# Kernel optimization log

Measured on AMD Instinct MI355X. Metric: run time of the kernel, lower is better.

## Reference

```python
import jax, jax.numpy as jnp
import numpy as np

NEG_INF = -1e9  # module uses -1e9 negativeInfinity constant
BS, DA, SL, H = 16, 512, 1024, 8


def setup_inputs() -> dict:
    key = jax.random.key(0)
    ks = jax.random.split(key, 8)
    return {
        "q":    jax.random.normal(ks[0], (BS, DA, SL), dtype=jnp.float32),
        "k_in": jax.random.normal(ks[1], (BS, DA, SL), dtype=jnp.float32),
        "v_in": jax.random.normal(ks[2], (BS, DA, SL), dtype=jnp.float32),
        "k_w":  jax.random.normal(ks[3], (DA, DA), dtype=jnp.float32) * 0.05,
        "k_b":  jax.random.normal(ks[4], (DA,), dtype=jnp.float32) * 0.05,
        "v_w":  jax.random.normal(ks[5], (DA, DA), dtype=jnp.float32) * 0.05,
        "v_b":  jax.random.normal(ks[6], (DA,), dtype=jnp.float32) * 0.05,
        "gbn_gamma": jnp.ones((H,), dtype=jnp.float32),
        "gbn_bias":  jnp.zeros((H,), dtype=jnp.float32),
        "gbn_m":     jnp.zeros((H,), dtype=jnp.float32),
        "gbn_s":     jnp.ones((H,), dtype=jnp.float32),
        "mask": jax.random.randint(ks[7], (BS, 1, 1, SL), 0, 2, dtype=jnp.int32),
    }


def reference(q, k_in, v_in, k_w, k_b, v_w, v_b, gbn_gamma, gbn_bias, gbn_m, gbn_s, mask):
    bs, da, qsl = q.shape
    h = gbn_gamma.shape[0]
    dh = da // h
    sl = k_in.shape[2]
    mask_b = mask.astype(bool)                 # [bs,1,1,sl] True = masked

    # 1x1 conv1d projections == per-position matmul over channels
    k = jnp.einsum('ok,bks->bos', k_w, k_in) + k_b[None, :, None]   # [bs,da,sl]
    v = jnp.einsum('ov,bvs->bos', v_w, v_in) + v_b[None, :, None]   # [bs,dva,sl]
    dva = v.shape[1]
    dvh = dva // h

    qh = q.reshape(bs, h, dh, qsl).transpose(0, 1, 3, 2)   # [bs,h,qsl,dh]
    kh = k.reshape(bs, h, dh, sl)                          # [bs,h,dh,sl]
    vh = v.reshape(bs, h, dvh, sl).transpose(0, 1, 3, 2)   # [bs,h,sl,dvh]

    scores = jnp.einsum('bhqd,bhds->bhqs', qh, kh)         # [bs,h,qsl,sl]

    # GhostBatchNorm1d(features=h) in eval mode: per-head affine normalization
    scores = (scores - gbn_m[None, :, None, None]) / gbn_s[None, :, None, None]
    scores = scores * gbn_gamma[None, :, None, None] + gbn_bias[None, :, None, None]

    mask_k = mask_b                           # [bs,1,1,sl]  mask key positions (selfAttention fill)
    mask_q = jnp.swapaxes(mask_b, 2, 3)       # [bs,1,sl,1]  mask query rows (transposed fill)
    scores = jnp.where(mask_k, NEG_INF, scores)
    scores = jnp.where(mask_q, NEG_INF, scores)

    w = jax.nn.softmax(scores, axis=-1)
    w = jnp.where(mask_q, 0.0, w)             # v_weights.masked_fill(mask, 0)

    out = jnp.einsum('bhqs,bhsd->bhqd', w, vh)             # [bs,h,qsl,dvh]
    out = out.transpose(0, 1, 3, 2).reshape(bs, dva, qsl)  # back to channels-first
    return out
```

## Files before the change

kernel.cpp:

```cpp
#include <hip/hip_runtime.h>

typedef _Float16 f16;
typedef _Float16 h8_t __attribute__((ext_vector_type(8)));
typedef _Float16 h4_t __attribute__((ext_vector_type(4)));
typedef float f32x4 __attribute__((ext_vector_type(4)));
typedef float f32x16 __attribute__((ext_vector_type(16)));

#define BS 16
#define DA 512
#define SL 1024
#define NH 8
#define DH 64

__device__ __forceinline__ void gload_lds16(const void* g, void* l) {
  __builtin_amdgcn_global_load_lds((const __attribute__((address_space(1))) void*)g,
                                   (__attribute__((address_space(3))) void*)l, 16, 0, 0);
}

__global__ __launch_bounds__(256) void prep_kernel(
    const float* __restrict__ k_in, const float* __restrict__ v_in,
    const float* __restrict__ k_w, const float* __restrict__ v_w,
    f16* __restrict__ Kt, f16* __restrict__ Vt,
    f16* __restrict__ kwh, f16* __restrict__ vwh) {
  const int blk = blockIdx.x;
  const int t = threadIdx.x;
  if (blk < 2048) {
    const int which = blk >> 10;
    const int r = blk & 1023;
    const int b = r >> 6;
    const int c0 = ((r >> 3) & 7) * 64;
    const int s0 = (r & 7) * 128;
    const float* src = which ? v_in : k_in;
    f16* dst = which ? Vt : Kt;
    __shared__ __align__(16) float Xf32[64 * 132];
#pragma unroll
    for (int p = 0; p < 8; ++p) {
      const int idx = p * 256 + t;
      const int cc = idx >> 5, s4 = (idx & 31) * 4;
      const float4 v = *(const float4*)&src[((size_t)b * DA + c0 + cc) * SL + s0 + s4];
      *(float4*)&Xf32[cc * 132 + s4] = v;
    }
    __syncthreads();
    const int srow = t >> 1, cb = (t & 1) * 32;
#pragma unroll
    for (int g = 0; g < 4; ++g) {
      h8_t h;
#pragma unroll
      for (int u = 0; u < 8; ++u) h[u] = (f16)Xf32[(cb + g * 8 + u) * 132 + srow];
      *(h8_t*)&dst[((size_t)b * SL + s0 + srow) * DA + c0 + cb + g * 8] = h;
    }
  } else {
    const int r = blk - 2048;
    const int wsel = r >> 5;
    const float* src = wsel ? v_w : k_w;
    f16* dst = wsel ? vwh : kwh;
    const int base = (r & 31) * 8192;
#pragma unroll
    for (int p = 0; p < 4; ++p) {
      const int i = base + p * 2048 + t * 8;
      const float4 a = *(const float4*)&src[i];
      const float4 c = *(const float4*)&src[i + 4];
      h8_t h;
      h[0] = (f16)a.x; h[1] = (f16)a.y; h[2] = (f16)a.z; h[3] = (f16)a.w;
      h[4] = (f16)c.x; h[5] = (f16)c.y; h[6] = (f16)c.z; h[7] = (f16)c.w;
      *(h8_t*)&dst[i] = h;
    }
  }
}

__global__ __launch_bounds__(256, 4) void proj_gemm_all(
    const f16* __restrict__ kwh, const f16* __restrict__ vwh,
    const f16* __restrict__ Kt, const f16* __restrict__ Vt,
    const float* __restrict__ k_b, const float* __restrict__ v_b,
    f16* __restrict__ kp, f16* __restrict__ vp) {
  __shared__ __align__(16) f16 LD[2][8192];
  const int mode = blockIdx.z;
  const int b = blockIdx.y;
  const int tx = blockIdx.x;
  const int m0 = (mode ? (tx >> 2) : (tx & 3)) * 128;
  const int n0 = (mode ? (tx & 3) : (tx >> 2)) * 128;
  const int t = threadIdx.x;
  const int lane = t & 63, w = t >> 6, lr = lane & 15, lq = lane >> 4;
  const int wm = (w >> 1) * 64, wn = (w & 1) * 64;

  const f16* Arow = (mode ? Vt + (size_t)b * SL * DA : kwh) + (size_t)m0 * DA;
  const f16* Brow = (mode ? vwh : Kt + (size_t)b * SL * DA) + (size_t)n0 * DA;

  const int rr = t >> 2;
  const int c8 = (t & 3) * 8;
  const int lo8 = t * 8;

  const f16* ga0 = Arow + (size_t)rr * DA + c8;
  const f16* ga1 = Arow + (size_t)(64 + rr) * DA + c8;
  const f16* gb0 = Brow + (size_t)rr * DA + c8;
  const f16* gb1 = Brow + (size_t)(64 + rr) * DA + c8;

  f32x4 acc[4][4] = {};

  gload_lds16(ga0, &LD[0][0] + lo8);
  gload_lds16(ga1, &LD[0][2048] + lo8);
  gload_lds16(gb0, &LD[0][4096] + lo8);
  gload_lds16(gb1, &LD[0][6144] + lo8);
  ga0 += 32; ga1 += 32; gb0 += 32; gb1 += 32;

  for (int kt = 0; kt < 16; ++kt) {
    const int cur = kt & 1;
    if (kt < 15) {
      f16* nb = &LD[cur ^ 1][0];
      gload_lds16(ga0, nb + lo8);
      gload_lds16(ga1, nb + 2048 + lo8);
      gload_lds16(gb0, nb + 4096 + lo8);
      gload_lds16(gb1, nb + 6144 + lo8);
      ga0 += 32; ga1 += 32; gb0 += 32; gb1 += 32;
      asm volatile("s_waitcnt vmcnt(4)" ::: "memory");
    } else {
      asm volatile("s_waitcnt vmcnt(0)" ::: "memory");
    }
    __builtin_amdgcn_s_barrier();
    __builtin_amdgcn_sched_barrier(0);

    const f16* Al = &LD[cur][0];
    const f16* Bl = &LD[cur][4096];
    h8_t af[4], bf[4];
#pragma unroll
    for (int i = 0; i < 4; ++i) af[i] = *(const h8_t*)&Al[(wm + i * 16 + lr) * 32 + lq * 8];
#pragma unroll
    for (int j = 0; j < 4; ++j) bf[j] = *(const h8_t*)&Bl[(wn + j * 16 + lr) * 32 + lq * 8];
    __builtin_amdgcn_s_setprio(1);
#pragma unroll
    for (int i = 0; i < 4; ++i)
#pragma unroll
      for (int j = 0; j < 4; ++j)
        acc[i][j] = __builtin_amdgcn_mfma_f32_16x16x32_f16(af[i], bf[j], acc[i][j], 0, 0, 0);
    __builtin_amdgcn_s_setprio(0);

    if (kt < 15) {
      __builtin_amdgcn_sched_barrier(0);
      __builtin_amdgcn_s_barrier();
      __builtin_amdgcn_sched_barrier(0);
    }
  }

#pragma unroll
  for (int i = 0; i < 4; ++i) {
    const int gmb = m0 + wm + i * 16 + lq * 4;
    float bm[4] = {0.f, 0.f, 0.f, 0.f};
    if (mode == 0) {
      const float4 b4 = *(const float4*)&k_b[gmb];
      bm[0] = b4.x; bm[1] = b4.y; bm[2] = b4.z; bm[3] = b4.w;
    }
#pragma unroll
    for (int j = 0; j < 4; ++j) {
      const int gn = n0 + wn + j * 16 + lr;
      const float bn = mode ? v_b[gn] : 0.f;
      h4_t hv;
#pragma unroll
      for (int r = 0; r < 4; ++r) {
        const float val = acc[i][j][r] + (mode == 0 ? bm[r] : bn);
        hv[r] = (f16)val;
      }
      f16* dst = mode ? &vp[((size_t)b * DA + gn) * SL + gmb]
                      : &kp[((size_t)b * SL + gn) * DA + gmb];
      *(h4_t*)dst = hv;
    }
  }
}

template <int MODE>
__global__ __launch_bounds__(256) void fused_proj(const float* __restrict__ Wg,
                                                  const float* __restrict__ Xin,
                                                  const float* __restrict__ bias,
                                                  f16* __restrict__ outg) {
  constexpr int MT = MODE ? SL : DA;
  constexpr int NT = MODE ? DA : SL;
  __shared__ f16 Wl[128 * 40];
  __shared__ f16 Xl[128 * 40];
  __shared__ float Xf32[32 * 132];
  const int b = blockIdx.z;
  const int m0 = blockIdx.x * 128;
  const int n0 = blockIdx.y * 128;
  const int o_base = MODE ? n0 : m0;
  const int s_base = MODE ? m0 : n0;
  const int t = threadIdx.x;
  const int w = t >> 6, lane = t & 63, lr = lane & 15, lq = lane >> 4;
  const int wm = (w >> 1) * 64, wn = (w & 1) * 64;

  f32x4 acc[4][4] = {};

  for (int kt = 0; kt < 16; ++kt) {
    const int c0 = kt * 32;
    __syncthreads();
#pragma unroll
    for (int p = 0; p < 4; ++p) {
      const int idx = p * 256 + t;
      const int row = idx >> 3, cq = (idx & 7) * 4;
      const float4 v = *(const float4*)&Wg[(size_t)(o_base + row) * DA + c0 + cq];
      h4_t hv;
      hv[0] = (f16)v.x; hv[1] = (f16)v.y; hv[2] = (f16)v.z; hv[3] = (f16)v.w;
      *(h4_t*)&Wl[row * 40 + cq] = hv;
    }
#pragma unroll
    for (int p = 0; p < 4; ++p) {
      const int idx = p * 256 + t;
      const int cc = idx >> 5, s4 = (idx & 31) * 4;
      const float4 v = *(const float4*)&Xin[((size_t)b * DA + c0 + cc) * SL + s_base + s4];
      *(float4*)&Xf32[cc * 132 + s4] = v;
    }
    __syncthreads();
    {
      const int srow = t >> 1, cb = (t & 1) * 16;
      h8_t lo, hi;
#pragma unroll
      for (int u = 0; u < 8; ++u) lo[u] = (f16)Xf32[(cb + u) * 132 + srow];
#pragma unroll
      for (int u = 0; u < 8; ++u) hi[u] = (f16)Xf32[(cb + 8 + u) * 132 + srow];
      *(h8_t*)&Xl[srow * 40 + cb] = lo;
      *(h8_t*)&Xl[srow * 40 + cb + 8] = hi;
    }
    __syncthreads();
    const f16* Alp = MODE ? Xl : Wl;
    const f16* Blp = MODE ? Wl : Xl;
    h8_t af[4], bf[4];
#pragma unroll
    for (int i = 0; i < 4; ++i) af[i] = *(const h8_t*)&Alp[(wm + i * 16 + lr) * 40 + lq * 8];
#pragma unroll
    for (int j = 0; j < 4; ++j) bf[j] = *(const h8_t*)&Blp[(wn + j * 16 + lr) * 40 + lq * 8];
#pragma unroll
    for (int i = 0; i < 4; ++i)
#pragma unroll
      for (int j = 0; j < 4; ++j)
        acc[i][j] = __builtin_amdgcn_mfma_f32_16x16x32_f16(af[i], bf[j], acc[i][j], 0, 0, 0);
  }

#pragma unroll
  for (int i = 0; i < 4; ++i) {
    const int gmb = m0 + wm + i * 16 + lq * 4;
    float bm[4] = {0.f, 0.f, 0.f, 0.f};
    if (MODE == 0) {
      const float4 b4 = *(const float4*)&bias[gmb];
      bm[0] = b4.x; bm[1] = b4.y; bm[2] = b4.z; bm[3] = b4.w;
    }
#pragma unroll
    for (int j = 0; j < 4; ++j) {
      const int gn = n0 + wn + j * 16 + lr;
      const float bn = (MODE == 1) ? bias[gn] : 0.f;
      h4_t hv;
#pragma unroll
      for (int r = 0; r < 4; ++r) {
        const float val = acc[i][j][r] + (MODE == 0 ? bm[r] : bn);
        hv[r] = (f16)val;
      }
      *(h4_t*)&outg[((size_t)b * NT + gn) * MT + gmb] = hv;
    }
  }
}

__global__ __launch_bounds__(512, 4) void attn_kernel(
    const float* __restrict__ qg, const f16* __restrict__ kp, const f16* __restrict__ vp,
    const float* __restrict__ gamma, const float* __restrict__ gbns,
    const int* __restrict__ maskg, float* __restrict__ outg) {
  __shared__ __align__(16) char smem[36864 + 4096];
  f16* KV = (f16*)smem;
  float* Osh = (float*)smem;
  float* biasf = (float*)(smem + 36864);

  const int bh = blockIdx.x, b = bh >> 3, h = bh & 7;
  const int i0 = blockIdx.y * 256;
  const int t = threadIdx.x, w = t >> 6, lane = t & 63;
  const int l5 = lane & 31, hf = lane >> 5;
  const float scale = gamma[h] / gbns[h] * 1.44269504088896f;
  const int iw = i0 + w * 32 + l5;

  h8_t qf[4];
#pragma unroll
  for (int ks = 0; ks < 4; ++ks) {
    h8_t v;
#pragma unroll
    for (int u = 0; u < 8; ++u) {
      const int d = ks * 16 + hf * 8 + u;
      v[u] = (f16)(qg[((size_t)b * DA + h * DH + d) * SL + iw] * scale);
    }
    qf[ks] = v;
  }

  {
    const int2 m2 = *(const int2*)&maskg[b * SL + t * 2];
    biasf[t * 2 + 0] = m2.x ? -1e9f : 0.f;
    biasf[t * 2 + 1] = m2.y ? -1e9f : 0.f;
  }

  const int srow = t >> 3;
  const int c8 = (t & 7) * 8;

  uint4 rk = *(const uint4*)&kp[((size_t)b * SL + srow) * DA + h * DH + c8];
  uint4 rv = *(const uint4*)&vp[((size_t)b * DA + h * DH + srow) * SL + c8];
  {
    f16* K0 = KV;
    f16* V0 = KV + 4608;
    const int rowp = (srow & ~12) | ((srow & 4) << 1) | ((srow & 8) >> 1);
    *(uint4*)&K0[rowp * 72 + c8] = rk;
    *(uint4*)&V0[srow * 72 + c8] = rv;
  }
  __syncthreads();

  float m_i = -3e38f, l_i = 0.f;
  f32x16 acc[2] = {};

  for (int jt = 0; jt < 16; ++jt) {
    const int j0 = jt * 64;
    const f16* Kc = KV + (jt & 1) * 9216;
    const f16* Vc = Kc + 4608;

    if (jt < 15) {
      const int jn = j0 + 64;
      rk = *(const uint4*)&kp[((size_t)b * SL + jn + srow) * DA + h * DH + c8];
      rv = *(const uint4*)&vp[((size_t)b * DA + h * DH + srow) * SL + jn + c8];
    }

    f32x16 sa[2] = {};
    __builtin_amdgcn_s_setprio(1);
#pragma unroll
    for (int ks = 0; ks < 4; ++ks)
#pragma unroll
      for (int mj = 0; mj < 2; ++mj) {
        const h8_t kf = *(const h8_t*)&Kc[(mj * 32 + l5) * 72 + ks * 16 + hf * 8];
        sa[mj] = __builtin_amdgcn_mfma_f32_32x32x16_f16(kf, qf[ks], sa[mj], 0, 0, 0);
      }
    __builtin_amdgcn_s_setprio(0);

#pragma unroll
    for (int mj = 0; mj < 2; ++mj)
#pragma unroll
      for (int qq = 0; qq < 4; ++qq) {
        const float4 bq = *(const float4*)&biasf[j0 + mj * 32 + (qq >> 1) * 16 + hf * 8 + (qq & 1) * 4];
        sa[mj][qq * 4 + 0] += bq.x;
        sa[mj][qq * 4 + 1] += bq.y;
        sa[mj][qq * 4 + 2] += bq.z;
        sa[mj][qq * 4 + 3] += bq.w;
      }

    {
      float a[8];
#pragma unroll
      for (int u = 0; u < 8; ++u)
        a[u] = fmaxf(fmaxf(sa[0][u], sa[0][u + 8]), fmaxf(sa[1][u], sa[1][u + 8]));
      float mx = fmaxf(fmaxf(fmaxf(a[0], a[1]), fmaxf(a[2], a[3])),
                       fmaxf(fmaxf(a[4], a[5]), fmaxf(a[6], a[7])));
      mx = fmaxf(mx, __shfl_xor(mx, 32));
      if (!__all(mx - m_i <= 8.0f)) {
        const float mn = fmaxf(m_i, mx);
        const float alpha = __builtin_amdgcn_exp2f(m_i - mn);
        m_i = mn;
        l_i *= alpha;
#pragma unroll
        for (int nd = 0; nd < 2; ++nd)
#pragma unroll
          for (int e = 0; e < 16; ++e) acc[nd][e] *= alpha;
      }
      float r0 = 0.f, r1 = 0.f, r2 = 0.f, r3 = 0.f;
#pragma unroll
      for (int mj = 0; mj < 2; ++mj)
#pragma unroll
        for (int e = 0; e < 16; e += 4) {
          const float p0 = __builtin_amdgcn_exp2f(sa[mj][e + 0] - m_i);
          const float p1 = __builtin_amdgcn_exp2f(sa[mj][e + 1] - m_i);
          const float p2 = __builtin_amdgcn_exp2f(sa[mj][e + 2] - m_i);
          const float p3 = __builtin_amdgcn_exp2f(sa[mj][e + 3] - m_i);
          sa[mj][e + 0] = p0; sa[mj][e + 1] = p1;
          sa[mj][e + 2] = p2; sa[mj][e + 3] = p3;
          r0 += p0; r1 += p1; r2 += p2; r3 += p3;
        }
      float rs = (r0 + r1) + (r2 + r3);
      rs += __shfl_xor(rs, 32);
      l_i += rs;
    }

    __builtin_amdgcn_s_setprio(1);
#pragma unroll
    for (int jk = 0; jk < 4; ++jk) {
      const int mj = jk >> 1, g = jk & 1;
      h8_t pk;
#pragma unroll
      for (int u = 0; u < 8; ++u) pk[u] = (f16)sa[mj][g * 8 + u];
#pragma unroll
      for (int nd = 0; nd < 2; ++nd) {
        const h8_t vf = *(const h8_t*)&Vc[(nd * 32 + l5) * 72 + jk * 16 + hf * 8];
        acc[nd] = __builtin_amdgcn_mfma_f32_32x32x16_f16(vf, pk, acc[nd], 0, 0, 0);
      }
    }
    __builtin_amdgcn_s_setprio(0);

    if (jt < 15) {
      f16* Kn = KV + ((jt + 1) & 1) * 9216;
      f16* Vn = Kn + 4608;
      const int rowp = (srow & ~12) | ((srow & 4) << 1) | ((srow & 8) >> 1);
      *(uint4*)&Kn[rowp * 72 + c8] = rk;
      *(uint4*)&Vn[srow * 72 + c8] = rv;
      __syncthreads();
    }
  }

  const int mo = maskg[b * SL + iw];
  const float fac = mo ? 0.f : 1.f / l_i;
  __syncthreads();

#pragma unroll
  for (int nd = 0; nd < 2; ++nd) {
#pragma unroll
    for (int e = 0; e < 16; ++e) {
      const int dl = (e & 3) + 8 * (e >> 2) + 4 * hf;
      Osh[dl * 256 + w * 32 + l5] = acc[nd][e] * fac;
    }
    __syncthreads();
#pragma unroll
    for (int pass = 0; pass < 4; ++pass) {
      const int row = pass * 8 + (t >> 6);
      const int i4 = (t & 63) * 4;
      const float4 o = *(const float4*)&Osh[row * 256 + i4];
      *(float4*)&outg[((size_t)b * DA + h * DH + nd * 32 + row) * SL + i0 + i4] = o;
    }
    __syncthreads();
  }
}

extern "C" void kernel_launch(void* const* d_in, const int* in_sizes, int n_in,
                              void* d_out, int out_size, void* d_ws, size_t ws_size,
                              hipStream_t stream) {
  const float* q     = (const float*)d_in[0];
  const float* k_in  = (const float*)d_in[1];
  const float* v_in  = (const float*)d_in[2];
  const float* k_w   = (const float*)d_in[3];
  const float* k_b   = (const float*)d_in[4];
  const float* v_w   = (const float*)d_in[5];
  const float* v_b   = (const float*)d_in[6];
  const float* gamma = (const float*)d_in[7];
  const float* gbns  = (const float*)d_in[10];
  const int*   mask  = (const int*)d_in[11];
  float* out = (float*)d_out;

  const size_t NEL = (size_t)BS * SL * DA;
  f16* kpw = (f16*)d_ws;
  f16* vpw = kpw + NEL;

  const size_t need = NEL * 2 * 4 + (size_t)DA * DA * 2 * 2;
  if (ws_size >= need) {
    f16* Kt  = vpw + NEL;
    f16* Vt  = Kt + NEL;
    f16* kwh = Vt + NEL;
    f16* vwh = kwh + (size_t)DA * DA;
    prep_kernel<<<dim3(2112), 256, 0, stream>>>(k_in, v_in, k_w, v_w, Kt, Vt, kwh, vwh);
    proj_gemm_all<<<dim3(32, BS, 2), 256, 0, stream>>>(kwh, vwh, Kt, Vt, k_b, v_b, kpw, vpw);
  } else {
    fused_proj<0><<<dim3(4, 8, BS), 256, 0, stream>>>(k_w, k_in, k_b, kpw);
    fused_proj<1><<<dim3(8, 4, BS), 256, 0, stream>>>(v_w, v_in, v_b, vpw);
  }
  attn_kernel<<<dim3(BS * NH, SL / 256), 512, 0, stream>>>(q, kpw, vpw, gamma, gbns, mask, out);
}
```

Baseline: 235.0 us.

## Fold key mask bias into QK MFMA via padding column, interleave exp with PV

The key-mask bias is no longer staged as a separate fp32 LDS array and added element by element. It is written as an fp16 value (-30000 or 0) into the padding column 64 of each K row, and an extra MFMA with a one-hot Q fragment adds it into the scores. The exp2 and row-sum computation is moved into the PV loop so it interleaves with the PV MFMAs and the packing to fp16. This cuts LDS traffic and VALU adds but costs two extra MFMAs per tile, an extra mask load, a zeroing pass with one more barrier, and relies on -30000 in fp16 underflowing exp2 the same way -1e9 did.

```diff
diff --git a/kernel.cpp b/kernel.cpp
--- a/kernel.cpp
+++ b/kernel.cpp
@@ -259,10 +259,9 @@
     const float* __restrict__ qg, const f16* __restrict__ kp, const f16* __restrict__ vp,
     const float* __restrict__ gamma, const float* __restrict__ gbns,
     const int* __restrict__ maskg, float* __restrict__ outg) {
-  __shared__ __align__(16) char smem[36864 + 4096];
+  __shared__ __align__(16) char smem[36864];
   f16* KV = (f16*)smem;
   float* Osh = (float*)smem;
-  float* biasf = (float*)(smem + 36864);
 
   const int bh = blockIdx.x, b = bh >> 3, h = bh & 7;
   const int i0 = blockIdx.y * 256;
@@ -282,24 +281,31 @@
     }
     qf[ks] = v;
   }
-
-  {
-    const int2 m2 = *(const int2*)&maskg[b * SL + t * 2];
-    biasf[t * 2 + 0] = m2.x ? -1e9f : 0.f;
-    biasf[t * 2 + 1] = m2.y ? -1e9f : 0.f;
-  }
+  h8_t qf5;
+#pragma unroll
+  for (int u = 0; u < 8; ++u) qf5[u] = (f16)0.f;
+  if (hf == 0) qf5[0] = (f16)1.f;
 
   const int srow = t >> 3;
   const int c8 = (t & 7) * 8;
 
   uint4 rk = *(const uint4*)&kp[((size_t)b * SL + srow) * DA + h * DH + c8];
   uint4 rv = *(const uint4*)&vp[((size_t)b * DA + h * DH + srow) * SL + c8];
+  int mbn = maskg[b * SL + srow];
+
+  if (t < 128) {
+    const int zr = t & 63, zb = t >> 6;
+    uint4 z; z.x = 0; z.y = 0; z.z = 0; z.w = 0;
+    *(uint4*)&KV[zb * 9216 + zr * 72 + 64] = z;
+  }
+  __syncthreads();
   {
     f16* K0 = KV;
     f16* V0 = KV + 4608;
     const int rowp = (srow & ~12) | ((srow & 4) << 1) | ((srow & 8) >> 1);
     *(uint4*)&K0[rowp * 72 + c8] = rk;
     *(uint4*)&V0[srow * 72 + c8] = rv;
+    if ((t & 7) == 0) K0[rowp * 72 + 64] = mbn ? (f16)(-30000.f) : (f16)0.f;
   }
   __syncthreads();
 
@@ -315,6 +321,7 @@
       const int jn = j0 + 64;
       rk = *(const uint4*)&kp[((size_t)b * SL + jn + srow) * DA + h * DH + c8];
       rv = *(const uint4*)&vp[((size_t)b * DA + h * DH + srow) * SL + jn + c8];
+      mbn = maskg[b * SL + jn + srow];
     }
 
     f32x16 sa[2] = {};
@@ -326,18 +333,12 @@
         const h8_t kf = *(const h8_t*)&Kc[(mj * 32 + l5) * 72 + ks * 16 + hf * 8];
         sa[mj] = __builtin_amdgcn_mfma_f32_32x32x16_f16(kf, qf[ks], sa[mj], 0, 0, 0);
       }
+#pragma unroll
+    for (int mj = 0; mj < 2; ++mj) {
+      const h8_t kf5 = *(const h8_t*)&Kc[(mj * 32 + l5) * 72 + 64];
+      sa[mj] = __builtin_amdgcn_mfma_f32_32x32x16_f16(kf5, qf5, sa[mj], 0, 0, 0);
+    }
     __builtin_amdgcn_s_setprio(0);
-
-#pragma unroll
-    for (int mj = 0; mj < 2; ++mj)
-#pragma unroll
-      for (int qq = 0; qq < 4; ++qq) {
-        const float4 bq = *(const float4*)&biasf[j0 + mj * 32 + (qq >> 1) * 16 + hf * 8 + (qq & 1) * 4];
-        sa[mj][qq * 4 + 0] += bq.x;
-        sa[mj][qq * 4 + 1] += bq.y;
-        sa[mj][qq * 4 + 2] += bq.z;
-        sa[mj][qq * 4 + 3] += bq.w;
-      }
 
     {
       float a[8];
@@ -357,31 +358,25 @@
 #pragma unroll
           for (int e = 0; e < 16; ++e) acc[nd][e] *= alpha;
       }
-      float r0 = 0.f, r1 = 0.f, r2 = 0.f, r3 = 0.f;
-#pragma unroll
-      for (int mj = 0; mj < 2; ++mj)
-#pragma unroll
-        for (int e = 0; e < 16; e += 4) {
-          const float p0 = __builtin_amdgcn_exp2f(sa[mj][e + 0] - m_i);
-          const float p1 = __builtin_amdgcn_exp2f(sa[mj][e + 1] - m_i);
-          const float p2 = __builtin_amdgcn_exp2f(sa[mj][e + 2] - m_i);
-          const float p3 = __builtin_amdgcn_exp2f(sa[mj][e + 3] - m_i);
-          sa[mj][e + 0] = p0; sa[mj][e + 1] = p1;
-          sa[mj][e + 2] = p2; sa[mj][e + 3] = p3;
-          r0 += p0; r1 += p1; r2 += p2; r3 += p3;
-        }
-      float rs = (r0 + r1) + (r2 + r3);
-      rs += __shfl_xor(rs, 32);
-      l_i += rs;
-    }
-
+    }
+
+    float r0 = 0.f, r1 = 0.f, r2 = 0.f, r3 = 0.f;
     __builtin_amdgcn_s_setprio(1);
 #pragma unroll
     for (int jk = 0; jk < 4; ++jk) {
       const int mj = jk >> 1, g = jk & 1;
+      float p0 = __builtin_amdgcn_exp2f(sa[mj][g * 8 + 0] - m_i);
+      float p1 = __builtin_amdgcn_exp2f(sa[mj][g * 8 + 1] - m_i);
+      float p2 = __builtin_amdgcn_exp2f(sa[mj][g * 8 + 2] - m_i);
+      float p3 = __builtin_amdgcn_exp2f(sa[mj][g * 8 + 3] - m_i);
+      float p4 = __builtin_amdgcn_exp2f(sa[mj][g * 8 + 4] - m_i);
+      float p5 = __builtin_amdgcn_exp2f(sa[mj][g * 8 + 5] - m_i);
+      float p6 = __builtin_amdgcn_exp2f(sa[mj][g * 8 + 6] - m_i);
+      float p7 = __builtin_amdgcn_exp2f(sa[mj][g * 8 + 7] - m_i);
       h8_t pk;
-#pragma unroll
-      for (int u = 0; u < 8; ++u) pk[u] = (f16)sa[mj][g * 8 + u];
+      pk[0] = (f16)p0; pk[1] = (f16)p1; pk[2] = (f16)p2; pk[3] = (f16)p3;
+      pk[4] = (f16)p4; pk[5] = (f16)p5; pk[6] = (f16)p6; pk[7] = (f16)p7;
+      r0 += p0 + p4; r1 += p1 + p5; r2 += p2 + p6; r3 += p3 + p7;
 #pragma unroll
       for (int nd = 0; nd < 2; ++nd) {
         const h8_t vf = *(const h8_t*)&Vc[(nd * 32 + l5) * 72 + jk * 16 + hf * 8];
@@ -389,6 +384,11 @@
       }
     }
     __builtin_amdgcn_s_setprio(0);
+    {
+      float rs = (r0 + r1) + (r2 + r3);
+      rs += __shfl_xor(rs, 32);
+      l_i += rs;
+    }
 
     if (jt < 15) {
       f16* Kn = KV + ((jt + 1) & 1) * 9216;
@@ -396,6 +396,7 @@
       const int rowp = (srow & ~12) | ((srow & 4) << 1) | ((srow & 8) >> 1);
       *(uint4*)&Kn[rowp * 72 + c8] = rk;
       *(uint4*)&Vn[srow * 72 + c8] = rv;
+      if ((t & 7) == 0) Kn[rowp * 72 + 64] = mbn ? (f16)(-30000.f) : (f16)0.f;
       __syncthreads();
     }
   }
```

After: 236.8 us. Within noise of the previous version (+0.8%).
